# Performance work log

Hardware: AMD Instinct MI355X
Metric: run time of the kernel (lower is better)

The kernel has to match this reference:

```python
import jax, jax.numpy as jnp
import numpy as np

B, S, D = 4, 256, 768      # batch, seq, activation_dim
F = 8192                   # dict_size (both modules)
K = 64                     # topk
C = 128                    # connections per downstream feature


def _topk_keep(post, k):
    """Keep top-k entries per row, zero elsewhere. post: [N, F]."""
    vals, idx = jax.lax.top_k(post, k)
    n = post.shape[0]
    return jnp.zeros_like(post).at[jnp.arange(n)[:, None], idx].set(vals)


def setup_inputs() -> dict:
    key = jax.random.key(0)
    ks = jax.random.split(key, 10)
    s = 1.0 / np.sqrt(D)
    return {
        "initial_acts": jax.random.normal(ks[0], (B, S, D), jnp.float32),
        "x_up": jax.random.normal(ks[1], (B, S, D), jnp.float32),
        "ln_scale": jax.random.uniform(ks[2], (B, S), jnp.float32, 0.5, 1.5),
        "W_enc_up": jax.random.normal(ks[3], (F, D), jnp.float32) * s,
        "b_enc_up": jnp.zeros((F,), jnp.float32),
        "W_dec_up": jax.random.normal(ks[4], (D, F), jnp.float32) * s,
        "b_dec_up": jax.random.normal(ks[5], (D,), jnp.float32) * 0.01,
        "W_enc_down": jax.random.normal(ks[6], (F, D), jnp.float32) * s,
        "b_enc_down": jnp.zeros((F,), jnp.float32),
        "W_dec_down": jax.random.normal(ks[7], (D, F), jnp.float32) * s,
        "b_dec_down": jax.random.normal(ks[8], (D,), jnp.float32) * 0.01,
        "conn": jax.random.randint(ks[9], (F, C), 0, F),  # all valid (no -1 pad)
    }


def reference(initial_acts, x_up, ln_scale,
              W_enc_up, b_enc_up, W_dec_up, b_dec_up,
              W_enc_down, b_enc_down, W_dec_down, b_dec_down,
              conn):
    b, s, d = initial_acts.shape
    n = b * s
    x0 = initial_acts.reshape(n, d)
    xu = x_up.reshape(n, d)
    ln = ln_scale.reshape(n)

    # --- vanilla_forward on upstream: TopK SAE encode + decode ---
    post_up = jax.nn.relu((xu - b_dec_up) @ W_enc_up.T + b_enc_up)  # [n, F]
    feat_up = _topk_keep(post_up, K)
    recon_up = feat_up @ W_dec_up.T + b_dec_up                      # [n, d]

    # --- pruned downstream path ---
    fd = W_enc_down.shape[0]
    fu = W_dec_up.shape[1]
    # virtual weights: down_encoder @ up_decoder  -> [F_down, F_up]
    virtual = W_enc_down @ W_dec_up
    # connection mask from index tensor [F_down, C]
    mask = jnp.zeros((fd, fu), bool).at[jnp.arange(fd)[:, None], conn].set(True)
    masked = jnp.where(mask, virtual, jnp.zeros((), virtual.dtype))

    approx = x0 @ W_enc_down.T                                      # initial contributions [n, F_down]
    approx = approx + feat_up @ masked.T + W_enc_down @ b_dec_up    # pruned contributions + b_dec term
    approx = approx / ln[:, None] + b_enc_down - W_enc_down @ b_dec_down

    feat_down = _topk_keep(approx, K)
    recon_down = feat_down @ W_dec_down.T + b_dec_down              # [n, d]

    return jnp.stack([recon_up.reshape(b, s, d), recon_down.reshape(b, s, d)])
```

## Files before the change

kernel.cpp:

```cpp
#include <hip/hip_runtime.h>


#define NTOK 1024
#define DIM  768
#define FF   8192
#define KK   64
#define CC   128
#define KSEL_UP 80
#define KSEL_DN 96
#define CAP  128

typedef unsigned short u16;
typedef unsigned int   u32;
typedef __attribute__((ext_vector_type(8))) short short8;
typedef __attribute__((ext_vector_type(4))) float floatx4;

__device__ __forceinline__ float bits2f(u32 v) {
    float f; __builtin_memcpy(&f, &v, 4); return f;
}
__device__ __forceinline__ float bf2f(u16 u) { return bits2f(((u32)u) << 16); }
__device__ __forceinline__ u16 f2bf(float f) {
    u32 u; __builtin_memcpy(&u, &f, 4);
    u32 lsb = (u >> 16) & 1u;
    u += 0x7fffu + lsb;
    return (u16)(u >> 16);
}
__device__ __forceinline__ u32 f2key(float x) {
    u32 u; __builtin_memcpy(&u, &x, 4);
    return (u & 0x80000000u) ? ~u : (u | 0x80000000u);
}

__global__ __launch_bounds__(256) void convert_kernel(const float* __restrict__ src,
                                                      u16* __restrict__ dst, int n4) {
    int i = blockIdx.x * 256 + threadIdx.x;
    if (i < n4) {
        float4 v = ((const float4*)src)[i];
        ushort4 o;
        o.x = f2bf(v.x); o.y = f2bf(v.y); o.z = f2bf(v.z); o.w = f2bf(v.w);
        ((ushort4*)dst)[i] = o;
    }
}

__global__ __launch_bounds__(256) void transpose_kernel(const float* __restrict__ in,
                                                        float* __restrict__ out) {
    __shared__ float tile[32][33];
    int f0 = blockIdx.x * 32, d0 = blockIdx.y * 32;
    int tx = threadIdx.x, ty = threadIdx.y;
#pragma unroll
    for (int i = 0; i < 4; ++i)
        tile[ty + 8 * i][tx] = in[(size_t)(d0 + ty + 8 * i) * FF + f0 + tx];
    __syncthreads();
#pragma unroll
    for (int i = 0; i < 4; ++i)
        out[(size_t)(f0 + ty + 8 * i) * DIM + d0 + tx] = tile[tx][ty + 8 * i];
}

__global__ __launch_bounds__(64) void bias_kernel(const float* __restrict__ Weu,
                                                  const float* __restrict__ Wed,
                                                  const float* __restrict__ bdu,
                                                  const float* __restrict__ bdd,
                                                  float* __restrict__ sF,
                                                  float* __restrict__ tuF,
                                                  float* __restrict__ tdF,
                                                  double* __restrict__ s64,
                                                  double* __restrict__ tu64,
                                                  double* __restrict__ td64) {
    int f = blockIdx.x, lane = threadIdx.x;
    double su = 0.0, tu = 0.0, td = 0.0;
    for (int i = lane; i < DIM; i += 64) {
        double bu = (double)bdu[i], bd = (double)bdd[i];
        su += (double)Weu[(size_t)f * DIM + i] * bu;
        double w = (double)Wed[(size_t)f * DIM + i];
        tu += w * bu;
        td += w * bd;
    }
#pragma unroll
    for (int off = 32; off; off >>= 1) {
        su += __shfl_xor(su, off);
        tu += __shfl_xor(tu, off);
        td += __shfl_xor(td, off);
    }
    if (lane == 0) {
        sF[f] = (float)su; tuF[f] = (float)tu; tdF[f] = (float)td;
        s64[f] = su; tu64[f] = tu; td64[f] = td;
    }
}

template <int MODE>
__global__ __launch_bounds__(256) void gemm_mfma(const u16* __restrict__ A16,
                                                 const u16* __restrict__ B16,
                                                 u16* __restrict__ Xout,
                                                 const float* __restrict__ sF,
                                                 const float* __restrict__ b_enc) {
    __shared__ __align__(16) u16 As[128 * 40];
    __shared__ __align__(16) u16 Bs[128 * 40];
    int tid = threadIdx.x;
    int wave = tid >> 6, lane = tid & 63;
    int lm = lane & 15, quad = lane >> 4;
    int m0 = blockIdx.y * 128, n0 = blockIdx.x * 128;
    int wm = (wave >> 1) * 64, wn = (wave & 1) * 64;
    floatx4 acc[4][4];
#pragma unroll
    for (int i = 0; i < 4; ++i)
#pragma unroll
        for (int j = 0; j < 4; ++j)
            acc[i][j] = (floatx4){0.f, 0.f, 0.f, 0.f};
    int r = tid >> 2;
    int s = (tid & 3) * 8;
    const u16* gA = A16 + (size_t)(m0 + r) * DIM + s;
    const u16* gB = B16 + (size_t)(n0 + r) * DIM + s;
    for (int k0 = 0; k0 < DIM; k0 += 32) {
        __syncthreads();
        *(int4*)&As[r * 40 + s]          = *(const int4*)(gA + k0);
        *(int4*)&As[(r + 64) * 40 + s]   = *(const int4*)(gA + (size_t)64 * DIM + k0);
        *(int4*)&Bs[r * 40 + s]          = *(const int4*)(gB + k0);
        *(int4*)&Bs[(r + 64) * 40 + s]   = *(const int4*)(gB + (size_t)64 * DIM + k0);
        __syncthreads();
        short8 af[4], bfr[4];
#pragma unroll
        for (int mi = 0; mi < 4; ++mi)
            af[mi] = *(const short8*)&As[(wm + mi * 16 + lm) * 40 + quad * 8];
#pragma unroll
        for (int ni = 0; ni < 4; ++ni)
            bfr[ni] = *(const short8*)&Bs[(wn + ni * 16 + lm) * 40 + quad * 8];
#pragma unroll
        for (int mi = 0; mi < 4; ++mi)
#pragma unroll
            for (int ni = 0; ni < 4; ++ni)
                acc[mi][ni] = __builtin_amdgcn_mfma_f32_16x16x32_bf16(
                    af[mi], bfr[ni], acc[mi][ni], 0, 0, 0);
    }
#pragma unroll
    for (int ni = 0; ni < 4; ++ni) {
        int col = n0 + wn + ni * 16 + lm;
        float sub = 0.f, bb = 0.f;
        if (MODE == 0) { sub = sF[col]; bb = b_enc[col]; }
#pragma unroll
        for (int mi = 0; mi < 4; ++mi) {
#pragma unroll
            for (int reg = 0; reg < 4; ++reg) {
                int row = m0 + wm + mi * 16 + quad * 4 + reg;
                float v = acc[mi][ni][reg];
                if (MODE == 0) { v = v - sub + bb; v = v > 0.f ? v : 0.f; }
                Xout[(size_t)row * FF + col] = f2bf(v);
            }
        }
    }
}

__global__ __launch_bounds__(256) void select_up_kernel(const u16* __restrict__ X16,
                                                        u16* __restrict__ cand,
                                                        int* __restrict__ cnt) {
    __shared__ float xr[FF];
    __shared__ u32 hist[256];
    __shared__ u32 sh_prefix;
    __shared__ int sh_k;
    __shared__ u32 sh_cntG, sh_cntE;
    __shared__ int eqidx[256];
    const int rrow = blockIdx.x, tid = threadIdx.x;
    const ushort4* src = (const ushort4*)(X16 + (size_t)rrow * FF);
    for (int i = tid; i < FF / 4; i += 256) {
        ushort4 u = src[i];
        xr[i * 4]     = bf2f(u.x);
        xr[i * 4 + 1] = bf2f(u.y);
        xr[i * 4 + 2] = bf2f(u.z);
        xr[i * 4 + 3] = bf2f(u.w);
    }
    if (tid == 0) { sh_prefix = 0; sh_k = KSEL_UP; }
    __syncthreads();
    for (int pass = 0; pass < 4; ++pass) {
        hist[tid] = 0;
        __syncthreads();
        u32 prefix = sh_prefix;
        int shift = 24 - 8 * pass;
        for (int i = tid; i < FF; i += 256) {
            u32 key = f2key(xr[i]);
            if (pass == 0 || (key >> (shift + 8)) == prefix)
                atomicAdd(&hist[(key >> shift) & 255u], 1u);
        }
        __syncthreads();
        if (tid == 0) {
            int rem = sh_k;
            int b = 255;
            for (; b > 0; --b) {
                int h = (int)hist[b];
                if (rem <= h) break;
                rem -= h;
            }
            sh_prefix = (prefix << 8) | (u32)b;
            sh_k = rem;
        }
        __syncthreads();
    }
    u32 T = sh_prefix;
    if (tid == 0) { sh_cntG = 0; sh_cntE = 0; }
    __syncthreads();
    u16* cr = cand + (size_t)rrow * CAP;
    for (int i = tid; i < FF; i += 256) {
        u32 key = f2key(xr[i]);
        if (key > T) {
            u32 p = atomicAdd(&sh_cntG, 1u);
            if (p < CAP) cr[p] = (u16)i;
        } else if (key == T) {
            u32 p = atomicAdd(&sh_cntE, 1u);
            if (p < 256) eqidx[p] = i;
        }
    }
    __syncthreads();
    if (tid == 0) {
        int G = (int)sh_cntG; if (G > CAP) G = CAP;
        int ne = (int)sh_cntE; if (ne > 256) ne = 256;
        int total = G;
        for (int q = 0; q < ne && total < CAP; ++q) cr[total++] = (u16)eqidx[q];
        cnt[rrow] = total;
    }
}

__device__ __forceinline__ bool sort_before(double av, int ai, double bv, int bi) {
    return (av > bv) || (av == bv && ai < bi);
}
__device__ void bitonic128(double* sv, int* si, int tid) {
    for (int k = 2; k <= 128; k <<= 1) {
        for (int j = k >> 1; j > 0; j >>= 1) {
            __syncthreads();
            if (tid < 64) {
                int i = ((tid & ~(j - 1)) << 1) | (tid & (j - 1));
                int l = i, rr = i + j;
                bool bfirst = sort_before(sv[rr], si[rr], sv[l], si[l]);
                bool doswap = ((i & k) == 0) ? bfirst : !bfirst;
                if (doswap) {
                    double tv = sv[l]; sv[l] = sv[rr]; sv[rr] = tv;
                    int ti = si[l]; si[l] = si[rr]; si[rr] = ti;
                }
            }
        }
    }
    __syncthreads();
}

__global__ __launch_bounds__(256) void fixup_up(const float* __restrict__ xu,
                                                const float* __restrict__ Weu,
                                                const double* __restrict__ s64,
                                                const float* __restrict__ beu,
                                                const u16* __restrict__ cand,
                                                const int* __restrict__ cnt,
                                                float* __restrict__ vals,
                                                int* __restrict__ idxs) {
    __shared__ float xrow[DIM];
    __shared__ double sv[128];
    __shared__ int si[128];
    int t = blockIdx.x, tid = threadIdx.x, wave = tid >> 6, lane = tid & 63;
    for (int i = tid; i < DIM; i += 256) xrow[i] = xu[(size_t)t * DIM + i];
    for (int c = tid; c < 128; c += 256) { sv[c] = -1.0e300; si[c] = 0x7fffffff; }
    __syncthreads();
    int nc = cnt[t]; if (nc > 128) nc = 128;
    for (int c = wave; c < nc; c += 4) {
        int f = (int)cand[(size_t)t * CAP + c];
        const float* wr = Weu + (size_t)f * DIM;
        double p = 0.0;
#pragma unroll
        for (int i = 0; i < 12; ++i) {
            int d = lane + 64 * i;
            p += (double)xrow[d] * (double)wr[d];
        }
#pragma unroll
        for (int off = 32; off; off >>= 1) p += __shfl_xor(p, off);
        if (lane == 0) {
            double v = p - s64[f] + (double)beu[f];
            v = v > 0.0 ? v : 0.0;
            sv[c] = v; si[c] = f;
        }
    }
    __syncthreads();
    bitonic128(sv, si, tid);
    if (tid < KK) {
        vals[(size_t)t * KK + tid] = (float)sv[tid];
        idxs[(size_t)t * KK + tid] = si[tid];
    }
}

__global__ __launch_bounds__(256) void fixup_dn(const float* __restrict__ x0,
                                                const float* __restrict__ Wed,
                                                const float* __restrict__ WduT,
                                                const double* __restrict__ tu64,
                                                const double* __restrict__ td64,
                                                const float* __restrict__ bed,
                                                const float* __restrict__ ln,
                                                const u16* __restrict__ cclean,
                                                const float* __restrict__ vals_up,
                                                const int* __restrict__ idx_up,
                                                const u16* __restrict__ cand,
                                                const int* __restrict__ cnt,
                                                float* __restrict__ vals,
                                                int* __restrict__ idxs) {
    __shared__ float xrow[DIM];
    __shared__ u32 bm[256];
    __shared__ int fl[KK];
    __shared__ float zl[KK];
    __shared__ double sv[128];
    __shared__ int si[128];
    int t = blockIdx.x, tid = threadIdx.x, wave = tid >> 6, lane = tid & 63;
    for (int i = tid; i < DIM; i += 256) xrow[i] = x0[(size_t)t * DIM + i];
    if (tid < 256) bm[tid] = 0;
    for (int c = tid; c < 128; c += 256) { sv[c] = -1.0e300; si[c] = 0x7fffffff; }
    __syncthreads();
    if (tid < KK) {
        int f = idx_up[(size_t)t * KK + tid];
        fl[tid] = f; zl[tid] = vals_up[(size_t)t * KK + tid];
        atomicOr(&bm[f >> 5], 1u << (f & 31));
    }
    __syncthreads();
    int nc = cnt[t]; if (nc > 128) nc = 128;
    double lnt = (double)ln[t];
    for (int c = wave; c < nc; c += 4) {
        int f = (int)cand[(size_t)t * CAP + c];
        const float* wr = Wed + (size_t)f * DIM;
        double p = 0.0;
#pragma unroll
        for (int i = 0; i < 12; ++i) {
            int d = lane + 64 * i;
            p += (double)xrow[d] * (double)wr[d];
        }
        const u16* crow = cclean + (size_t)f * CC;
        int e0 = (int)crow[lane], e1 = (int)crow[lane + 64];
        bool h0 = (e0 != 0xFFFF) && ((bm[e0 >> 5] >> (e0 & 31)) & 1u);
        bool h1 = (e1 != 0xFFFF) && ((bm[e1 >> 5] >> (e1 & 31)) & 1u);
        unsigned long long m0 = __ballot(h0), m1 = __ballot(h1);
        while (m0 | m1) {
            int fu;
            if (m0) {
                int b = __ffsll((long long)m0) - 1; m0 &= m0 - 1;
                fu = __shfl(e0, b);
            } else {
                int b = __ffsll((long long)m1) - 1; m1 &= m1 - 1;
                fu = __shfl(e1, b);
            }
            unsigned long long zm = __ballot(fl[lane & 63] == fu && lane < KK);
            float z = zl[__ffsll((long long)zm) - 1];
            const float* du = WduT + (size_t)fu * DIM;
            double vp = 0.0;
#pragma unroll
            for (int i = 0; i < 12; ++i) {
                int d = lane + 64 * i;
                vp += (double)wr[d] * (double)du[d];
            }
            p += (double)z * vp;
        }
#pragma unroll
        for (int off = 32; off; off >>= 1) p += __shfl_xor(p, off);
        if (lane == 0) {
            double v = (p + tu64[f]) / lnt + (double)bed[f] - td64[f];
            sv[c] = v; si[c] = f;
        }
    }
    __syncthreads();
    bitonic128(sv, si, tid);
    if (tid < KK) {
        vals[(size_t)t * KK + tid] = (float)sv[tid];
        idxs[(size_t)t * KK + tid] = si[tid];
    }
}

__global__ __launch_bounds__(128) void dedup_deg_kernel(const int* __restrict__ conn,
                                                        u32* __restrict__ deg) {
    __shared__ int row[CC];
    int fd = blockIdx.x, c = threadIdx.x;
    int v = conn[(size_t)fd * CC + c];
    row[c] = v;
    __syncthreads();
    bool dup = false;
    for (int j = 0; j < c; ++j) dup |= (row[j] == v);
    if (!dup) atomicAdd(&deg[v], 1u);
}

__global__ __launch_bounds__(256) void scan_kernel(const u32* __restrict__ deg,
                                                   u32* __restrict__ offs) {
    __shared__ u32 sdeg[FF];
    __shared__ u32 part[256];
    int tid = threadIdx.x;
    for (int i = tid; i < FF; i += 256) sdeg[i] = deg[i];
    __syncthreads();
    u32 s = 0;
    for (int j = 0; j < 32; ++j) s += sdeg[tid * 32 + j];
    part[tid] = s;
    __syncthreads();
    if (tid == 0) {
        u32 run = 0;
        for (int i = 0; i < 256; ++i) { u32 v = part[i]; part[i] = run; run += v; }
        offs[FF] = run;
    }
    __syncthreads();
    u32 run = part[tid];
    for (int j = 0; j < 32; ++j) { offs[tid * 32 + j] = run; run += sdeg[tid * 32 + j]; }
}

__global__ __launch_bounds__(128) void fill_kernel(const int* __restrict__ conn,
                                                   const u32* __restrict__ offs,
                                                   u32* __restrict__ cursor,
                                                   u16* __restrict__ inv_fd,
                                                   u16* __restrict__ cclean) {
    __shared__ int row[CC];
    int fd = blockIdx.x, c = threadIdx.x;
    int v = conn[(size_t)fd * CC + c];
    row[c] = v;
    __syncthreads();
    bool dup = false;
    for (int j = 0; j < c; ++j) dup |= (row[j] == v);
    cclean[(size_t)fd * CC + c] = dup ? (u16)0xFFFF : (u16)v;
    if (!dup) {
        u32 slot = atomicAdd(&cursor[v], 1u);
        inv_fd[offs[v] + slot] = (u16)fd;
    }
}

__global__ __launch_bounds__(256) void vconn_chunk(const u16* __restrict__ Wed16,
                                                   const float* __restrict__ WduT,
                                                   const u32* __restrict__ offs,
                                                   const u16* __restrict__ inv_fd,
                                                   u16* __restrict__ v_inv16,
                                                   int chunk, int first) {
    __shared__ float row[192];
    int fu = blockIdx.x, tid = threadIdx.x;
    if (tid < 192) row[tid] = WduT[(size_t)fu * DIM + chunk * 192 + tid];
    __syncthreads();
    u32 s = offs[fu], e = offs[fu + 1];
    int wave = tid >> 6, lane = tid & 63;
    int sub = lane >> 4, sl = lane & 15;
    for (u32 p0 = s + (u32)wave * 4; p0 < e; p0 += 16) {
        u32 p = p0 + (u32)sub;
        bool valid = p < e;
        float a = 0.f;
        if (valid) {
            int fd = (int)inv_fd[p];
            const u16* wr = Wed16 + (size_t)fd * DIM + chunk * 192;
#pragma unroll
            for (int i = 0; i < 12; ++i)
                a = fmaf(bf2f(wr[sl + 16 * i]), row[sl + 16 * i], a);
        }
        a += __shfl_xor(a, 1);
        a += __shfl_xor(a, 2);
        a += __shfl_xor(a, 4);
        a += __shfl_xor(a, 8);
        if (valid && sl == 0) {
            if (first) v_inv16[p] = f2bf(a);
            else       v_inv16[p] = f2bf(bf2f(v_inv16[p]) + a);
        }
    }
}

__global__ __launch_bounds__(256) void phase2sel(const u16* __restrict__ X16,
                                                 const float* __restrict__ vals_up,
                                                 const int* __restrict__ idx_up,
                                                 const u32* __restrict__ offs,
                                                 const u16* __restrict__ inv_fd,
                                                 const u16* __restrict__ v_inv16,
                                                 const float* __restrict__ tuF,
                                                 const float* __restrict__ tdF,
                                                 const float* __restrict__ bed,
                                                 const float* __restrict__ ln,
                                                 u16* __restrict__ cand,
                                                 int* __restrict__ cnt) {
    __shared__ float acc[FF];
    __shared__ float z[KK];
    __shared__ int fidx[KK];
    __shared__ u32 hist[256];
    __shared__ u32 sh_prefix;
    __shared__ int sh_k;
    __shared__ u32 sh_cntG, sh_cntE;
    __shared__ int eqidx[256];
    int t = blockIdx.x, tid = threadIdx.x;
    for (int i = tid; i < FF; i += 256) acc[i] = 0.f;
    if (tid < KK) { z[tid] = vals_up[(size_t)t * KK + tid]; fidx[tid] = idx_up[(size_t)t * KK + tid]; }
    if (tid == 0) { sh_prefix = 0; sh_k = KSEL_DN; }
    __syncthreads();
    for (int j = 0; j < KK; ++j) {
        float zj = z[j];
        int f = fidx[j];
        u32 s = offs[f], e = offs[f + 1];
        for (u32 p = s + tid; p < e; p += 256)
            atomicAdd(&acc[(int)inv_fd[p]], zj * bf2f(v_inv16[p]));
    }
    __syncthreads();
    float lnv = ln[t];
    const ushort4* xsrc = (const ushort4*)(X16 + (size_t)t * FF);
    for (int i = tid; i < FF / 4; i += 256) {
        ushort4 u = xsrc[i];
#pragma unroll
        for (int q = 0; q < 4; ++q) {
            int idx = i * 4 + q;
            float xv = bf2f(q == 0 ? u.x : q == 1 ? u.y : q == 2 ? u.z : u.w);
            float v = xv + acc[idx] + tuF[idx];
            acc[idx] = v / lnv + bed[idx] - tdF[idx];
        }
    }
    __syncthreads();
    for (int pass = 0; pass < 4; ++pass) {
        hist[tid] = 0;
        __syncthreads();
        u32 prefix = sh_prefix;
        int shift = 24 - 8 * pass;
        for (int i = tid; i < FF; i += 256) {
            u32 key = f2key(acc[i]);
            if (pass == 0 || (key >> (shift + 8)) == prefix)
                atomicAdd(&hist[(key >> shift) & 255u], 1u);
        }
        __syncthreads();
        if (tid == 0) {
            int rem = sh_k;
            int b = 255;
            for (; b > 0; --b) {
                int h = (int)hist[b];
                if (rem <= h) break;
                rem -= h;
            }
            sh_prefix = (prefix << 8) | (u32)b;
            sh_k = rem;
        }
        __syncthreads();
    }
    u32 T = sh_prefix;
    if (tid == 0) { sh_cntG = 0; sh_cntE = 0; }
    __syncthreads();
    u16* cr = cand + (size_t)t * CAP;
    for (int i = tid; i < FF; i += 256) {
        u32 key = f2key(acc[i]);
        if (key > T) {
            u32 p = atomicAdd(&sh_cntG, 1u);
            if (p < CAP) cr[p] = (u16)i;
        } else if (key == T) {
            u32 p = atomicAdd(&sh_cntE, 1u);
            if (p < 256) eqidx[p] = i;
        }
    }
    __syncthreads();
    if (tid == 0) {
        int G = (int)sh_cntG; if (G > CAP) G = CAP;
        int ne = (int)sh_cntE; if (ne > 256) ne = 256;
        int total = G;
        for (int q = 0; q < ne && total < CAP; ++q) cr[total++] = (u16)eqidx[q];
        cnt[t] = total;
    }
}

__global__ __launch_bounds__(256) void decode_kernel(const float* __restrict__ vals,
                                                     const int* __restrict__ idxs,
                                                     const float* __restrict__ WdT,
                                                     const float* __restrict__ b_dec,
                                                     float* __restrict__ outp) {
    __shared__ float z[KK];
    __shared__ int fidx[KK];
    int t = blockIdx.x, tid = threadIdx.x;
    if (tid < KK) { z[tid] = vals[(size_t)t * KK + tid]; fidx[tid] = idxs[(size_t)t * KK + tid]; }
    __syncthreads();
    float a0 = 0.f, a1 = 0.f, a2 = 0.f;
    for (int j = 0; j < KK; ++j) {
        const float* wr = WdT + (size_t)fidx[j] * DIM;
        float zj = z[j];
        a0 = fmaf(zj, wr[tid], a0);
        a1 = fmaf(zj, wr[tid + 256], a1);
        a2 = fmaf(zj, wr[tid + 512], a2);
    }
    outp[(size_t)t * DIM + tid]       = a0 + b_dec[tid];
    outp[(size_t)t * DIM + tid + 256] = a1 + b_dec[tid + 256];
    outp[(size_t)t * DIM + tid + 512] = a2 + b_dec[tid + 512];
}

extern "C" void kernel_launch(void* const* d_in, const int* in_sizes, int n_in,
                              void* d_out, int out_size, void* d_ws, size_t ws_size,
                              hipStream_t stream) {
    const float* x0  = (const float*)d_in[0];
    const float* xu  = (const float*)d_in[1];
    const float* ln  = (const float*)d_in[2];
    const float* Weu = (const float*)d_in[3];
    const float* beu = (const float*)d_in[4];
    const float* Wdu = (const float*)d_in[5];
    const float* bdu = (const float*)d_in[6];
    const float* Wed = (const float*)d_in[7];
    const float* bed = (const float*)d_in[8];
    const float* Wdd = (const float*)d_in[9];
    const float* bdd = (const float*)d_in[10];
    const int* conn = (const int*)d_in[11];
    float* out = (float*)d_out;

    char* w = (char*)d_ws;
    size_t off = 0;
    auto take = [&](size_t bytes) { char* p = w + off; off = (off + bytes + 255) & ~(size_t)255; return p; };
    u16*   X16     = (u16*)take((size_t)NTOK * FF * 2);
    u16*   B16     = (u16*)take((size_t)FF * DIM * 2);
    float* WddT    = (float*)X16;
    float* WduT    = (float*)take((size_t)FF * DIM * 4);
    u16*   A16     = (u16*)take((size_t)NTOK * DIM * 2);
    u16*   v_inv16 = (u16*)take((size_t)FF * CC * 2);
    u16*   inv_fd  = (u16*)take((size_t)FF * CC * 2);
    u16*   cclean  = (u16*)take((size_t)FF * CC * 2);
    u16*   cand_u  = (u16*)take((size_t)NTOK * CAP * 2);
    u16*   cand_d  = (u16*)take((size_t)NTOK * CAP * 2);
    int*   cnt_u   = (int*)take(NTOK * 4);
    int*   cnt_d   = (int*)take(NTOK * 4);
    float* vals_up = (float*)take((size_t)NTOK * KK * 4);
    int*   idx_up  = (int*)take((size_t)NTOK * KK * 4);
    float* vals_dn = (float*)take((size_t)NTOK * KK * 4);
    int*   idx_dn  = (int*)take((size_t)NTOK * KK * 4);
    float* sF      = (float*)take(FF * 4);
    float* tuF     = (float*)take(FF * 4);
    float* tdF     = (float*)take(FF * 4);
    double* s64    = (double*)take(FF * 8);
    double* tu64   = (double*)take(FF * 8);
    double* td64   = (double*)take(FF * 8);
    u32*   deg     = (u32*)take(FF * 4);
    u32*   cursor  = (u32*)take(FF * 4);
    u32*   offs    = (u32*)take((FF + 8) * 4);

    dim3 tgrid(FF / 32, DIM / 32), tblk(32, 8);
    dim3 ggrid(FF / 128, NTOK / 128);
    int nA4 = NTOK * DIM / 4, nB4 = FF * DIM / 4;

    transpose_kernel<<<tgrid, tblk, 0, stream>>>(Wdu, WduT);
    bias_kernel<<<FF, 64, 0, stream>>>(Weu, Wed, bdu, bdd, sF, tuF, tdF, s64, tu64, td64);
    hipMemsetAsync(deg, 0, 2 * FF * sizeof(u32), stream);
    dedup_deg_kernel<<<FF, CC, 0, stream>>>(conn, deg);
    scan_kernel<<<1, 256, 0, stream>>>(deg, offs);
    fill_kernel<<<FF, CC, 0, stream>>>(conn, offs, cursor, inv_fd, cclean);

    convert_kernel<<<(nA4 + 255) / 256, 256, 0, stream>>>(xu, A16, nA4);
    convert_kernel<<<(nB4 + 255) / 256, 256, 0, stream>>>(Weu, B16, nB4);
    gemm_mfma<0><<<ggrid, 256, 0, stream>>>(A16, B16, X16, sF, beu);
    select_up_kernel<<<NTOK, 256, 0, stream>>>(X16, cand_u, cnt_u);
    fixup_up<<<NTOK, 256, 0, stream>>>(xu, Weu, s64, beu, cand_u, cnt_u, vals_up, idx_up);

    convert_kernel<<<(nA4 + 255) / 256, 256, 0, stream>>>(x0, A16, nA4);
    convert_kernel<<<(nB4 + 255) / 256, 256, 0, stream>>>(Wed, B16, nB4);
    gemm_mfma<1><<<ggrid, 256, 0, stream>>>(A16, B16, X16, sF, beu);
    vconn_chunk<<<FF, 256, 0, stream>>>(B16, WduT, offs, inv_fd, v_inv16, 0, 1);
    vconn_chunk<<<FF, 256, 0, stream>>>(B16, WduT, offs, inv_fd, v_inv16, 1, 0);
    vconn_chunk<<<FF, 256, 0, stream>>>(B16, WduT, offs, inv_fd, v_inv16, 2, 0);
    vconn_chunk<<<FF, 256, 0, stream>>>(B16, WduT, offs, inv_fd, v_inv16, 3, 0);
    phase2sel<<<NTOK, 256, 0, stream>>>(X16, vals_up, idx_up, offs, inv_fd, v_inv16,
                                        tuF, tdF, bed, ln, cand_d, cnt_d);
    fixup_dn<<<NTOK, 256, 0, stream>>>(x0, Wed, WduT, tu64, td64, bed, ln, cclean,
                                       vals_up, idx_up, cand_d, cnt_d, vals_dn, idx_dn);

    decode_kernel<<<NTOK, 256, 0, stream>>>(vals_up, idx_up, WduT, bdu, out);
    transpose_kernel<<<tgrid, tblk, 0, stream>>>(Wdd, WddT);
    decode_kernel<<<NTOK, 256, 0, stream>>>(vals_dn, idx_dn, WddT, bdd,
                                            out + (size_t)NTOK * DIM);
}
```

Baseline: 856.0 us.

## Use 16-bit radix select, packed edge data, wider fixup blocks, fused decode

Replaces the four-pass 32-bit radix select with a two-pass select on bf16 keys held in shared memory, shared by the upstream and downstream select kernels. Packs the downstream index and virtual-weight bf16 value into one u32 per edge. phase2sel now flattens the scatter over all 64 active features instead of looping feature by feature, and folds b_enc_down minus the td term into one precomputed bias. The fixup kernels move to 512 threads so more candidates run in parallel, and the two decode launches merge into one. These aim to cut passes over each row, memory reads and launch count, at the cost of bf16-rounded keys for candidate selection (the fixup recomputes exact values).

Measured after the change: 880.7 us. 2.9% more time.

```diff
diff --git a/kernel.cpp b/kernel.cpp
--- a/kernel.cpp
+++ b/kernel.cpp
@@ -25,9 +25,8 @@
     u += 0x7fffu + lsb;
     return (u16)(u >> 16);
 }
-__device__ __forceinline__ u32 f2key(float x) {
-    u32 u; __builtin_memcpy(&u, &x, 4);
-    return (u & 0x80000000u) ? ~u : (u | 0x80000000u);
+__device__ __forceinline__ u16 bfkey(u16 b) {
+    return (b & 0x8000u) ? (u16)~b : (u16)(b | 0x8000u);
 }
 
 __global__ __launch_bounds__(256) void convert_kernel(const float* __restrict__ src,
@@ -59,9 +58,10 @@
                                                   const float* __restrict__ Wed,
                                                   const float* __restrict__ bdu,
                                                   const float* __restrict__ bdd,
+                                                  const float* __restrict__ bed,
                                                   float* __restrict__ sF,
                                                   float* __restrict__ tuF,
-                                                  float* __restrict__ tdF,
+                                                  float* __restrict__ c2F,
                                                   double* __restrict__ s64,
                                                   double* __restrict__ tu64,
                                                   double* __restrict__ td64) {
@@ -81,7 +81,8 @@
         td += __shfl_xor(td, off);
     }
     if (lane == 0) {
-        sF[f] = (float)su; tuF[f] = (float)tu; tdF[f] = (float)td;
+        sF[f] = (float)su; tuF[f] = (float)tu;
+        c2F[f] = (float)((double)bed[f] - td);
         s64[f] = su; tu64[f] = tu; td64[f] = td;
     }
 }
@@ -148,72 +149,76 @@
     }
 }
 
+__device__ void radix_collect_u16(const u16* keys, u32* hist, int* eqidx,
+                                  int ksel, u16* cr, int* cnt_out, int row,
+                                  u32* shG, u32* shE, int* shB, int* shK) {
+    int tid = threadIdx.x;
+    if (tid < 256) hist[tid] = 0;
+    __syncthreads();
+    for (int i = tid; i < FF; i += blockDim.x) atomicAdd(&hist[keys[i] >> 8], 1u);
+    __syncthreads();
+    if (tid == 0) {
+        int rem = ksel, b = 255;
+        for (; b > 0; --b) { int h = (int)hist[b]; if (rem <= h) break; rem -= h; }
+        *shB = b; *shK = rem;
+    }
+    __syncthreads();
+    int hb = *shB;
+    if (tid < 256) hist[tid] = 0;
+    __syncthreads();
+    for (int i = tid; i < FF; i += blockDim.x) {
+        u16 k = keys[i];
+        if ((int)(k >> 8) == hb) atomicAdd(&hist[k & 255u], 1u);
+    }
+    __syncthreads();
+    if (tid == 0) {
+        int rem = *shK, b = 255;
+        for (; b > 0; --b) { int h = (int)hist[b]; if (rem <= h) break; rem -= h; }
+        *shB = (hb << 8) | b;
+        *shG = 0; *shE = 0;
+    }
+    __syncthreads();
+    u16 T = (u16)*shB;
+    for (int i = tid; i < FF; i += blockDim.x) {
+        u16 k = keys[i];
+        if (k > T) {
+            u32 p = atomicAdd(shG, 1u);
+            if (p < CAP) cr[p] = (u16)i;
+        } else if (k == T) {
+            u32 p = atomicAdd(shE, 1u);
+            if (p < 256) eqidx[p] = i;
+        }
+    }
+    __syncthreads();
+    if (tid == 0) {
+        int G = (int)*shG; if (G > CAP) G = CAP;
+        int ne = (int)*shE; if (ne > 256) ne = 256;
+        int total = G;
+        for (int q = 0; q < ne && total < CAP; ++q) cr[total++] = (u16)eqidx[q];
+        cnt_out[row] = total;
+    }
+}
+
 __global__ __launch_bounds__(256) void select_up_kernel(const u16* __restrict__ X16,
                                                         u16* __restrict__ cand,
                                                         int* __restrict__ cnt) {
-    __shared__ float xr[FF];
+    __shared__ u16 keys[FF];
     __shared__ u32 hist[256];
-    __shared__ u32 sh_prefix;
-    __shared__ int sh_k;
-    __shared__ u32 sh_cntG, sh_cntE;
     __shared__ int eqidx[256];
-    const int rrow = blockIdx.x, tid = threadIdx.x;
-    const ushort4* src = (const ushort4*)(X16 + (size_t)rrow * FF);
+    __shared__ u32 shG, shE;
+    __shared__ int shB, shK;
+    const int row = blockIdx.x, tid = threadIdx.x;
+    const ushort4* src = (const ushort4*)(X16 + (size_t)row * FF);
     for (int i = tid; i < FF / 4; i += 256) {
         ushort4 u = src[i];
-        xr[i * 4]     = bf2f(u.x);
-        xr[i * 4 + 1] = bf2f(u.y);
-        xr[i * 4 + 2] = bf2f(u.z);
-        xr[i * 4 + 3] = bf2f(u.w);
-    }
-    if (tid == 0) { sh_prefix = 0; sh_k = KSEL_UP; }
-    __syncthreads();
-    for (int pass = 0; pass < 4; ++pass) {
-        hist[tid] = 0;
-        __syncthreads();
-        u32 prefix = sh_prefix;
-        int shift = 24 - 8 * pass;
-        for (int i = tid; i < FF; i += 256) {
-            u32 key = f2key(xr[i]);
-            if (pass == 0 || (key >> (shift + 8)) == prefix)
-                atomicAdd(&hist[(key >> shift) & 255u], 1u);
-        }
-        __syncthreads();
-        if (tid == 0) {
-            int rem = sh_k;
-            int b = 255;
-            for (; b > 0; --b) {
-                int h = (int)hist[b];
-                if (rem <= h) break;
-                rem -= h;
-            }
-            sh_prefix = (prefix << 8) | (u32)b;
-            sh_k = rem;
-        }
-        __syncthreads();
-    }
-    u32 T = sh_prefix;
-    if (tid == 0) { sh_cntG = 0; sh_cntE = 0; }
-    __syncthreads();
-    u16* cr = cand + (size_t)rrow * CAP;
-    for (int i = tid; i < FF; i += 256) {
-        u32 key = f2key(xr[i]);
-        if (key > T) {
-            u32 p = atomicAdd(&sh_cntG, 1u);
-            if (p < CAP) cr[p] = (u16)i;
-        } else if (key == T) {
-            u32 p = atomicAdd(&sh_cntE, 1u);
-            if (p < 256) eqidx[p] = i;
-        }
-    }
-    __syncthreads();
-    if (tid == 0) {
-        int G = (int)sh_cntG; if (G > CAP) G = CAP;
-        int ne = (int)sh_cntE; if (ne > 256) ne = 256;
-        int total = G;
-        for (int q = 0; q < ne && total < CAP; ++q) cr[total++] = (u16)eqidx[q];
-        cnt[rrow] = total;
-    }
+        keys[i * 4]     = bfkey(u.x);
+        keys[i * 4 + 1] = bfkey(u.y);
+        keys[i * 4 + 2] = bfkey(u.z);
+        keys[i * 4 + 3] = bfkey(u.w);
+    }
+    __syncthreads();
+    radix_collect_u16(keys, hist, eqidx, KSEL_UP, cand + (size_t)row * CAP, cnt, row,
+                      &shG, &shE, &shB, &shK);
 }
 
 __device__ __forceinline__ bool sort_before(double av, int ai, double bv, int bi) {
@@ -238,7 +243,7 @@
     __syncthreads();
 }
 
-__global__ __launch_bounds__(256) void fixup_up(const float* __restrict__ xu,
+__global__ __launch_bounds__(512) void fixup_up(const float* __restrict__ xu,
                                                 const float* __restrict__ Weu,
                                                 const double* __restrict__ s64,
                                                 const float* __restrict__ beu,
@@ -250,11 +255,11 @@
     __shared__ double sv[128];
     __shared__ int si[128];
     int t = blockIdx.x, tid = threadIdx.x, wave = tid >> 6, lane = tid & 63;
-    for (int i = tid; i < DIM; i += 256) xrow[i] = xu[(size_t)t * DIM + i];
-    for (int c = tid; c < 128; c += 256) { sv[c] = -1.0e300; si[c] = 0x7fffffff; }
+    for (int i = tid; i < DIM; i += 512) xrow[i] = xu[(size_t)t * DIM + i];
+    for (int c = tid; c < 128; c += 512) { sv[c] = -1.0e300; si[c] = 0x7fffffff; }
     __syncthreads();
     int nc = cnt[t]; if (nc > 128) nc = 128;
-    for (int c = wave; c < nc; c += 4) {
+    for (int c = wave; c < nc; c += 8) {
         int f = (int)cand[(size_t)t * CAP + c];
         const float* wr = Weu + (size_t)f * DIM;
         double p = 0.0;
@@ -279,7 +284,7 @@
     }
 }
 
-__global__ __launch_bounds__(256) void fixup_dn(const float* __restrict__ x0,
+__global__ __launch_bounds__(512) void fixup_dn(const float* __restrict__ x0,
                                                 const float* __restrict__ Wed,
                                                 const float* __restrict__ WduT,
                                                 const double* __restrict__ tu64,
@@ -300,9 +305,9 @@
     __shared__ double sv[128];
     __shared__ int si[128];
     int t = blockIdx.x, tid = threadIdx.x, wave = tid >> 6, lane = tid & 63;
-    for (int i = tid; i < DIM; i += 256) xrow[i] = x0[(size_t)t * DIM + i];
+    for (int i = tid; i < DIM; i += 512) xrow[i] = x0[(size_t)t * DIM + i];
     if (tid < 256) bm[tid] = 0;
-    for (int c = tid; c < 128; c += 256) { sv[c] = -1.0e300; si[c] = 0x7fffffff; }
+    for (int c = tid; c < 128; c += 512) { sv[c] = -1.0e300; si[c] = 0x7fffffff; }
     __syncthreads();
     if (tid < KK) {
         int f = idx_up[(size_t)t * KK + tid];
@@ -312,7 +317,7 @@
     __syncthreads();
     int nc = cnt[t]; if (nc > 128) nc = 128;
     double lnt = (double)ln[t];
-    for (int c = wave; c < nc; c += 4) {
+    for (int c = wave; c < nc; c += 8) {
         int f = (int)cand[(size_t)t * CAP + c];
         const float* wr = Wed + (size_t)f * DIM;
         double p = 0.0;
@@ -335,7 +340,7 @@
                 int b = __ffsll((long long)m1) - 1; m1 &= m1 - 1;
                 fu = __shfl(e1, b);
             }
-            unsigned long long zm = __ballot(fl[lane & 63] == fu && lane < KK);
+            unsigned long long zm = __ballot(fl[lane] == fu);
             float z = zl[__ffsll((long long)zm) - 1];
             const float* du = WduT + (size_t)fu * DIM;
             double vp = 0.0;
@@ -417,7 +422,7 @@
                                                    const float* __restrict__ WduT,
                                                    const u32* __restrict__ offs,
                                                    const u16* __restrict__ inv_fd,
-                                                   u16* __restrict__ v_inv16,
+                                                   u32* __restrict__ pe,
                                                    int chunk, int first) {
     __shared__ float row[192];
     int fu = blockIdx.x, tid = threadIdx.x;
@@ -430,8 +435,11 @@
         u32 p = p0 + (u32)sub;
         bool valid = p < e;
         float a = 0.f;
+        int fd = 0;
+        u32 old = 0;
         if (valid) {
-            int fd = (int)inv_fd[p];
+            if (first) fd = (int)inv_fd[p];
+            else { old = pe[p]; fd = (int)(old >> 16); }
             const u16* wr = Wed16 + (size_t)fd * DIM + chunk * 192;
 #pragma unroll
             for (int i = 0; i < 12; ++i)
@@ -442,8 +450,8 @@
         a += __shfl_xor(a, 4);
         a += __shfl_xor(a, 8);
         if (valid && sl == 0) {
-            if (first) v_inv16[p] = f2bf(a);
-            else       v_inv16[p] = f2bf(bf2f(v_inv16[p]) + a);
+            float v = first ? a : (bf2f((u16)(old & 0xffffu)) + a);
+            pe[p] = ((u32)fd << 16) | (u32)f2bf(v);
         }
     }
 }
@@ -452,104 +460,98 @@
                                                  const float* __restrict__ vals_up,
                                                  const int* __restrict__ idx_up,
                                                  const u32* __restrict__ offs,
-                                                 const u16* __restrict__ inv_fd,
-                                                 const u16* __restrict__ v_inv16,
+                                                 const u32* __restrict__ pe,
                                                  const float* __restrict__ tuF,
-                                                 const float* __restrict__ tdF,
-                                                 const float* __restrict__ bed,
+                                                 const float* __restrict__ c2F,
                                                  const float* __restrict__ ln,
                                                  u16* __restrict__ cand,
                                                  int* __restrict__ cnt) {
     __shared__ float acc[FF];
+    __shared__ u16 keys[FF];
+    __shared__ float zl[KK];
+    __shared__ u32 offs_s[KK];
+    __shared__ u32 cum[KK + 1];
+    __shared__ u32 hist[256];
+    __shared__ int eqidx[256];
+    __shared__ u32 shG, shE;
+    __shared__ int shB, shK;
+    int t = blockIdx.x, tid = threadIdx.x;
+    for (int i = tid; i < FF; i += 256) acc[i] = 0.f;
+    if (tid < KK) {
+        int f = idx_up[(size_t)t * KK + tid];
+        zl[tid] = vals_up[(size_t)t * KK + tid];
+        offs_s[tid] = offs[f];
+        cum[tid] = offs[f + 1] - offs[f];
+    }
+    __syncthreads();
+    if (tid == 0) {
+        u32 run = 0;
+        for (int j = 0; j < KK; ++j) { u32 d = cum[j]; cum[j] = run; run += d; }
+        cum[KK] = run;
+    }
+    __syncthreads();
+    u32 E = cum[KK];
+    for (u32 q0 = tid; q0 < E; q0 += 1024) {
+        u32 vv[4]; float zz[4];
+        int nv = 0;
+        u32 qq = q0;
+#pragma unroll
+        for (int u = 0; u < 4; ++u) {
+            if (qq < E) {
+                int j = 0;
+#pragma unroll
+                for (int b = 32; b; b >>= 1)
+                    if (j + b < KK && cum[j + b] <= qq) j += b;
+                u32 p = offs_s[j] + (qq - cum[j]);
+                vv[nv] = pe[p];
+                zz[nv] = zl[j];
+                ++nv;
+            }
+            qq += 256;
+        }
+        for (int u = 0; u < nv; ++u)
+            atomicAdd(&acc[vv[u] >> 16], zz[u] * bf2f((u16)(vv[u] & 0xffffu)));
+    }
+    __syncthreads();
+    float lnv = ln[t];
+    const ushort4* xs = (const ushort4*)(X16 + (size_t)t * FF);
+    for (int i = tid; i < FF / 4; i += 256) {
+        ushort4 u = xs[i];
+        float4 tu = ((const float4*)tuF)[i];
+        float4 c2 = ((const float4*)c2F)[i];
+        int i4 = i * 4;
+        float v0 = (bf2f(u.x) + acc[i4]     + tu.x) / lnv + c2.x;
+        float v1 = (bf2f(u.y) + acc[i4 + 1] + tu.y) / lnv + c2.y;
+        float v2 = (bf2f(u.z) + acc[i4 + 2] + tu.z) / lnv + c2.z;
+        float v3 = (bf2f(u.w) + acc[i4 + 3] + tu.w) / lnv + c2.w;
+        keys[i4]     = bfkey(f2bf(v0));
+        keys[i4 + 1] = bfkey(f2bf(v1));
+        keys[i4 + 2] = bfkey(f2bf(v2));
+        keys[i4 + 3] = bfkey(f2bf(v3));
+    }
+    __syncthreads();
+    radix_collect_u16(keys, hist, eqidx, KSEL_DN, cand + (size_t)t * CAP, cnt, t,
+                      &shG, &shE, &shB, &shK);
+}
+
+__global__ __launch_bounds__(256) void decode_both(const float* __restrict__ vals_up,
+                                                   const int* __restrict__ idx_up,
+                                                   const float* __restrict__ vals_dn,
+                                                   const int* __restrict__ idx_dn,
+                                                   const float* __restrict__ WduT,
+                                                   const float* __restrict__ WddT,
+                                                   const float* __restrict__ bdu,
+                                                   const float* __restrict__ bdd,
+                                                   float* __restrict__ outp) {
     __shared__ float z[KK];
     __shared__ int fidx[KK];
-    __shared__ u32 hist[256];
-    __shared__ u32 sh_prefix;
-    __shared__ int sh_k;
-    __shared__ u32 sh_cntG, sh_cntE;
-    __shared__ int eqidx[256];
-    int t = blockIdx.x, tid = threadIdx.x;
-    for (int i = tid; i < FF; i += 256) acc[i] = 0.f;
-    if (tid < KK) { z[tid] = vals_up[(size_t)t * KK + tid]; fidx[tid] = idx_up[(size_t)t * KK + tid]; }
-    if (tid == 0) { sh_prefix = 0; sh_k = KSEL_DN; }
-    __syncthreads();
-    for (int j = 0; j < KK; ++j) {
-        float zj = z[j];
-        int f = fidx[j];
-        u32 s = offs[f], e = offs[f + 1];
-        for (u32 p = s + tid; p < e; p += 256)
-            atomicAdd(&acc[(int)inv_fd[p]], zj * bf2f(v_inv16[p]));
-    }
-    __syncthreads();
-    float lnv = ln[t];
-    const ushort4* xsrc = (const ushort4*)(X16 + (size_t)t * FF);
-    for (int i = tid; i < FF / 4; i += 256) {
-        ushort4 u = xsrc[i];
-#pragma unroll
-        for (int q = 0; q < 4; ++q) {
-            int idx = i * 4 + q;
-            float xv = bf2f(q == 0 ? u.x : q == 1 ? u.y : q == 2 ? u.z : u.w);
-            float v = xv + acc[idx] + tuF[idx];
-            acc[idx] = v / lnv + bed[idx] - tdF[idx];
-        }
-    }
-    __syncthreads();
-    for (int pass = 0; pass < 4; ++pass) {
-        hist[tid] = 0;
-        __syncthreads();
-        u32 prefix = sh_prefix;
-        int shift = 24 - 8 * pass;
-        for (int i = tid; i < FF; i += 256) {
-            u32 key = f2key(acc[i]);
-            if (pass == 0 || (key >> (shift + 8)) == prefix)
-                atomicAdd(&hist[(key >> shift) & 255u], 1u);
-        }
-        __syncthreads();
-        if (tid == 0) {
-            int rem = sh_k;
-            int b = 255;
-            for (; b > 0; --b) {
-                int h = (int)hist[b];
-                if (rem <= h) break;
-                rem -= h;
-            }
-            sh_prefix = (prefix << 8) | (u32)b;
-            sh_k = rem;
-        }
-        __syncthreads();
-    }
-    u32 T = sh_prefix;
-    if (tid == 0) { sh_cntG = 0; sh_cntE = 0; }
-    __syncthreads();
-    u16* cr = cand + (size_t)t * CAP;
-    for (int i = tid; i < FF; i += 256) {
-        u32 key = f2key(acc[i]);
-        if (key > T) {
-            u32 p = atomicAdd(&sh_cntG, 1u);
-            if (p < CAP) cr[p] = (u16)i;
-        } else if (key == T) {
-            u32 p = atomicAdd(&sh_cntE, 1u);
-            if (p < 256) eqidx[p] = i;
-        }
-    }
-    __syncthreads();
-    if (tid == 0) {
-        int G = (int)sh_cntG; if (G > CAP) G = CAP;
-        int ne = (int)sh_cntE; if (ne > 256) ne = 256;
-        int total = G;
-        for (int q = 0; q < ne && total < CAP; ++q) cr[total++] = (u16)eqidx[q];
-        cnt[t] = total;
-    }
-}
-
-__global__ __launch_bounds__(256) void decode_kernel(const float* __restrict__ vals,
-                                                     const int* __restrict__ idxs,
-                                                     const float* __restrict__ WdT,
-                                                     const float* __restrict__ b_dec,
-                                                     float* __restrict__ outp) {
-    __shared__ float z[KK];
-    __shared__ int fidx[KK];
-    int t = blockIdx.x, tid = threadIdx.x;
+    int b = blockIdx.x, tid = threadIdx.x;
+    int which = b >> 10, t = b & 1023;
+    const float* vals = which ? vals_dn : vals_up;
+    const int* idxs = which ? idx_dn : idx_up;
+    const float* WdT = which ? WddT : WduT;
+    const float* bd = which ? bdd : bdu;
+    float* o = outp + (size_t)which * NTOK * DIM + (size_t)t * DIM;
     if (tid < KK) { z[tid] = vals[(size_t)t * KK + tid]; fidx[tid] = idxs[(size_t)t * KK + tid]; }
     __syncthreads();
     float a0 = 0.f, a1 = 0.f, a2 = 0.f;
@@ -560,9 +562,9 @@
         a1 = fmaf(zj, wr[tid + 256], a1);
         a2 = fmaf(zj, wr[tid + 512], a2);
     }
-    outp[(size_t)t * DIM + tid]       = a0 + b_dec[tid];
-    outp[(size_t)t * DIM + tid + 256] = a1 + b_dec[tid + 256];
-    outp[(size_t)t * DIM + tid + 512] = a2 + b_dec[tid + 512];
+    o[tid]       = a0 + bd[tid];
+    o[tid + 256] = a1 + bd[tid + 256];
+    o[tid + 512] = a2 + bd[tid + 512];
 }
 
 extern "C" void kernel_launch(void* const* d_in, const int* in_sizes, int n_in,
@@ -590,9 +592,9 @@
     float* WddT    = (float*)X16;
     float* WduT    = (float*)take((size_t)FF * DIM * 4);
     u16*   A16     = (u16*)take((size_t)NTOK * DIM * 2);
-    u16*   v_inv16 = (u16*)take((size_t)FF * CC * 2);
     u16*   inv_fd  = (u16*)take((size_t)FF * CC * 2);
     u16*   cclean  = (u16*)take((size_t)FF * CC * 2);
+    u32*   pe      = (u32*)take((size_t)FF * CC * 4);
     u16*   cand_u  = (u16*)take((size_t)NTOK * CAP * 2);
     u16*   cand_d  = (u16*)take((size_t)NTOK * CAP * 2);
     int*   cnt_u   = (int*)take(NTOK * 4);
@@ -603,7 +605,7 @@
     int*   idx_dn  = (int*)take((size_t)NTOK * KK * 4);
     float* sF      = (float*)take(FF * 4);
     float* tuF     = (float*)take(FF * 4);
-    float* tdF     = (float*)take(FF * 4);
+    float* c2F     = (float*)take(FF * 4);
     double* s64    = (double*)take(FF * 8);
     double* tu64   = (double*)take(FF * 8);
     double* td64   = (double*)take(FF * 8);
@@ -616,7 +618,8 @@
     int nA4 = NTOK * DIM / 4, nB4 = FF * DIM / 4;
 
     transpose_kernel<<<tgrid, tblk, 0, stream>>>(Wdu, WduT);
-    bias_kernel<<<FF, 64, 0, stream>>>(Weu, Wed, bdu, bdd, sF, tuF, tdF, s64, tu64, td64);
+    bias_kernel<<<FF, 64, 0, stream>>>(Weu, Wed, bdu, bdd, bed, sF, tuF, c2F,
+                                       s64, tu64, td64);
     hipMemsetAsync(deg, 0, 2 * FF * sizeof(u32), stream);
     dedup_deg_kernel<<<FF, CC, 0, stream>>>(conn, deg);
     scan_kernel<<<1, 256, 0, stream>>>(deg, offs);
@@ -626,22 +629,21 @@
     convert_kernel<<<(nB4 + 255) / 256, 256, 0, stream>>>(Weu, B16, nB4);
     gemm_mfma<0><<<ggrid, 256, 0, stream>>>(A16, B16, X16, sF, beu);
     select_up_kernel<<<NTOK, 256, 0, stream>>>(X16, cand_u, cnt_u);
-    fixup_up<<<NTOK, 256, 0, stream>>>(xu, Weu, s64, beu, cand_u, cnt_u, vals_up, idx_up);
+    fixup_up<<<NTOK, 512, 0, stream>>>(xu, Weu, s64, beu, cand_u, cnt_u, vals_up, idx_up);
 
     convert_kernel<<<(nA4 + 255) / 256, 256, 0, stream>>>(x0, A16, nA4);
     convert_kernel<<<(nB4 + 255) / 256, 256, 0, stream>>>(Wed, B16, nB4);
     gemm_mfma<1><<<ggrid, 256, 0, stream>>>(A16, B16, X16, sF, beu);
-    vconn_chunk<<<FF, 256, 0, stream>>>(B16, WduT, offs, inv_fd, v_inv16, 0, 1);
-    vconn_chunk<<<FF, 256, 0, stream>>>(B16, WduT, offs, inv_fd, v_inv16, 1, 0);
-    vconn_chunk<<<FF, 256, 0, stream>>>(B16, WduT, offs, inv_fd, v_inv16, 2, 0);
-    vconn_chunk<<<FF, 256, 0, stream>>>(B16, WduT, offs, inv_fd, v_inv16, 3, 0);
-    phase2sel<<<NTOK, 256, 0, stream>>>(X16, vals_up, idx_up, offs, inv_fd, v_inv16,
-                                        tuF, tdF, bed, ln, cand_d, cnt_d);
-    fixup_dn<<<NTOK, 256, 0, stream>>>(x0, Wed, WduT, tu64, td64, bed, ln, cclean,
+    vconn_chunk<<<FF, 256, 0, stream>>>(B16, WduT, offs, inv_fd, pe, 0, 1);
+    vconn_chunk<<<FF, 256, 0, stream>>>(B16, WduT, offs, inv_fd, pe, 1, 0);
+    vconn_chunk<<<FF, 256, 0, stream>>>(B16, WduT, offs, inv_fd, pe, 2, 0);
+    vconn_chunk<<<FF, 256, 0, stream>>>(B16, WduT, offs, inv_fd, pe, 3, 0);
+    phase2sel<<<NTOK, 256, 0, stream>>>(X16, vals_up, idx_up, offs, pe,
+                                        tuF, c2F, ln, cand_d, cnt_d);
+    fixup_dn<<<NTOK, 512, 0, stream>>>(x0, Wed, WduT, tu64, td64, bed, ln, cclean,
                                        vals_up, idx_up, cand_d, cnt_d, vals_dn, idx_dn);
 
-    decode_kernel<<<NTOK, 256, 0, stream>>>(vals_up, idx_up, WduT, bdu, out);
     transpose_kernel<<<tgrid, tblk, 0, stream>>>(Wdd, WddT);
-    decode_kernel<<<NTOK, 256, 0, stream>>>(vals_dn, idx_dn, WddT, bdd,
-                                            out + (size_t)NTOK * DIM);
-}
+    decode_both<<<2 * NTOK, 256, 0, stream>>>(vals_up, idx_up, vals_dn, idx_dn,
+                                              WduT, WddT, bdu, bdd, out);
+}
```
